# Kernel tuning notes

Measured on AMD Instinct MI355X. Metric: run time of the kernel, lower is better.

The kernel has to match this reference:

```python
import jax, jax.numpy as jnp
import numpy as np

H = 8    # num_heads (per-head feature size after the quirky split)
D_H = 16 # dim_heads (becomes the effective number of heads after split)


def _split_heads(x, B):
    # torch.split(x, H, dim=-1) then cat on dim 0: new_batch = chunk*B + b
    Bt, T, N, D = x.shape
    dh = D // H
    return x.reshape(B, T, N, dh, H).transpose(3, 0, 1, 2, 4).reshape(dh * B, T, N, H)


def _merge_heads(x, B):
    dhB, T, N, Hh = x.shape
    dh = dhB // B
    return x.reshape(dh, B, T, N, Hh).transpose(1, 2, 3, 0, 4).reshape(B, T, N, dh * Hh)


def setup_inputs() -> dict:
    key = jax.random.key(0)
    ks = jax.random.split(key, 10)
    B, T, N, D = 8, 64, 256, 128
    s_in = 1.0 / np.sqrt(2 * D)
    s_d = 1.0 / np.sqrt(D)
    return {
        "X": jax.random.normal(ks[0], (B, T, N, D), jnp.float32),
        "STE": jax.random.normal(ks[1], (B, T, N, D), jnp.float32),
        "Wq": jax.random.normal(ks[2], (2 * D, D), jnp.float32) * s_in,
        "bq": jnp.zeros((D,), jnp.float32),
        "Wk": jax.random.normal(ks[3], (2 * D, D), jnp.float32) * s_in,
        "bk": jnp.zeros((D,), jnp.float32),
        "Wv": jax.random.normal(ks[4], (2 * D, D), jnp.float32) * s_in,
        "bv": jnp.zeros((D,), jnp.float32),
        "Wo": jax.random.normal(ks[5], (D, D), jnp.float32) * s_d,
        "bo": jnp.zeros((D,), jnp.float32),
    }


def reference(X, STE, Wq, bq, Wk, bk, Wv, bv, Wo, bo):
    B, T, N, D = X.shape
    Xc = jnp.concatenate([X, STE], axis=-1)  # [B,T,N,2D]
    Q = jax.nn.relu(Xc @ Wq + bq)
    K = jax.nn.relu(Xc @ Wk + bk)
    V = jax.nn.relu(Xc @ Wv + bv)
    Q = _split_heads(Q, B)  # [dh*B, T, N, H]
    K = _split_heads(K, B)
    V = _split_heads(V, B)
    # scores over time per vertex: [dh*B, N, T, T]
    scores = jnp.einsum("btnh,bsnh->bnts", Q, K) / jnp.sqrt(jnp.float32(D_H))
    causal = jnp.tril(jnp.ones((T, T), bool))
    scores = jnp.where(causal, scores, -jnp.inf)
    attn = jax.nn.softmax(scores, axis=-1)
    out = jnp.einsum("bnts,bsnh->btnh", attn, V)  # [dh*B, T, N, H]
    out = _merge_heads(out, B)  # [B,T,N,D]
    return jax.nn.relu(out @ Wo + bo)
```

## Files before the change

### kernel.cpp

```cpp
#include <hip/hip_runtime.h>

using bf16x8  = __attribute__((ext_vector_type(8))) __bf16;
using f32x4   = __attribute__((ext_vector_type(4))) float;
using short8  = __attribute__((ext_vector_type(8))) short;
using float4v = __attribute__((ext_vector_type(4))) float;
using uint2v  = __attribute__((ext_vector_type(2))) unsigned int;

#if __has_builtin(__builtin_amdgcn_exp2f)
#define EXP2F(x) __builtin_amdgcn_exp2f(x)
#else
#define EXP2F(x) __expf((x) * 0.6931472f)
#endif
#if __has_builtin(__builtin_amdgcn_rcpf)
#define RCPF(x) __builtin_amdgcn_rcpf(x)
#else
#define RCPF(x) (1.f / (x))
#endif

static __device__ __forceinline__ unsigned short bfu(float f) {
    return __builtin_bit_cast(unsigned short, (__bf16)f);
}
static __device__ __forceinline__ unsigned int pkbf(float a, float b) {
    return (unsigned int)bfu(a) | ((unsigned int)bfu(b) << 16);
}
static __device__ __forceinline__ bf16x8 as_bf(short8 s) {
    return __builtin_bit_cast(bf16x8, s);
}

__global__ void prep_weights(const float* __restrict__ Wq, const float* __restrict__ Wk,
                             const float* __restrict__ Wv, const float* __restrict__ Wo,
                             unsigned short* __restrict__ wq2, unsigned short* __restrict__ wo2) {
    int idx = blockIdx.x * 256 + threadIdx.x;
    if (idx < 384 * 256) {
        int c = idx >> 8, k = idx & 255;
        float v = (c < 128) ? Wq[k * 128 + c]
                : (c < 256) ? Wk[k * 128 + (c - 128)]
                            : Wv[k * 128 + (c - 256)];
        wq2[(k >> 5) * 12288 + (c << 5) + (k & 31)] = bfu(v);
    } else {
        int j = idx - 384 * 256;
        int c = j >> 7, k = j & 127;
        wo2[(k >> 5) * 4096 + (c << 5) + (k & 31)] = bfu(Wo[k * 128 + c]);
    }
}

__global__ __launch_bounds__(256, 3)
void fused_attn(const float* __restrict__ X, const float* __restrict__ STE,
                const float* __restrict__ bq, const float* __restrict__ bk,
                const float* __restrict__ bv, const float* __restrict__ bo,
                const unsigned short* __restrict__ wq2, const unsigned short* __restrict__ wo2,
                float* __restrict__ out) {
    __shared__ __align__(16) char sm[49152];
    constexpr int SQ = 0, SK = 16384, SV = 32768;
    const float SC2 = 0.36067376f;

    const int tid  = threadIdx.x;
    const int lane = tid & 63;
    const int w    = tid >> 6;
    const int bid  = blockIdx.x;
    const int n    = bid & 255;
    const int b    = bid >> 8;
    const int lr   = lane & 15;
    const int lg   = lane >> 4;
    const int rsw  = (lr & 7) << 4;

    const size_t base = (size_t)(b * 16384 + n) * 128;
    const float* xbase = X   + base;
    const float* sbase = STE + base;

    const int c0 = w * 96;
    bf16x8 bnxt[6];
    #pragma unroll
    for (int i = 0; i < 6; ++i)
        bnxt[i] = as_bf(*reinterpret_cast<const short8*>(
            wq2 + (size_t)(c0 + i * 16 + lr) * 32 + lg * 8));

    #pragma unroll
    for (int it = 0; it < 16; ++it) {
        int t = w + it * 4;
        const float* src = (lane < 32) ? (xbase + (size_t)t * 32768 + lane * 4)
                                       : (sbase + (size_t)t * 32768 + (lane - 32) * 4);
        float4v v = *reinterpret_cast<const float4v*>(src);
        uint2v d;
        d[0] = pkbf(v[0], v[1]);
        d[1] = pkbf(v[2], v[3]);
        *reinterpret_cast<uint2v*>(sm + (t << 9) + ((lane * 8) ^ ((t & 7) << 4))) = d;
    }
    __syncthreads();

    f32x4 acc[4][6];
    #pragma unroll
    for (int m = 0; m < 4; ++m)
        #pragma unroll
        for (int i = 0; i < 6; ++i)
            acc[m][i] = f32x4{0.f, 0.f, 0.f, 0.f};

    #pragma unroll
    for (int ks = 0; ks < 8; ++ks) {
        bf16x8 bcur[6];
        #pragma unroll
        for (int i = 0; i < 6; ++i) bcur[i] = bnxt[i];
        if (ks < 7) {
            #pragma unroll
            for (int i = 0; i < 6; ++i)
                bnxt[i] = as_bf(*reinterpret_cast<const short8*>(
                    wq2 + (size_t)(ks + 1) * 12288 + (size_t)(c0 + i * 16 + lr) * 32 + lg * 8));
        }
        bf16x8 a[4];
        #pragma unroll
        for (int m = 0; m < 4; ++m)
            a[m] = as_bf(*reinterpret_cast<const short8*>(
                sm + ((m * 16 + lr) << 9) + ((ks * 64 + lg * 16) ^ rsw)));
        #pragma unroll
        for (int m = 0; m < 4; ++m)
            #pragma unroll
            for (int i = 0; i < 6; ++i)
                acc[m][i] = __builtin_amdgcn_mfma_f32_16x16x32_bf16(a[m], bcur[i], acc[m][i], 0, 0, 0);
    }
    __syncthreads();

    #pragma unroll
    for (int i = 0; i < 6; ++i) {
        int c = c0 + i * 16 + lr;
        if (c < 256) {
            int qi = c >> 7, cc = c & 127;
            char* rbase = sm + (qi ? SK : SQ);
            float bvv = (qi ? bk : bq)[cc];
            #pragma unroll
            for (int m = 0; m < 4; ++m)
                #pragma unroll
                for (int r = 0; r < 4; ++r) {
                    int t = m * 16 + lg * 4 + r;
                    *reinterpret_cast<unsigned short*>(
                        rbase + (t << 8) + ((cc * 2) ^ ((t & 7) << 4)))
                        = bfu(fmaxf(acc[m][i][r] + bvv, 0.f));
                }
        } else {
            int cv = c - 256;
            float bvv = bv[cv];
            #pragma unroll
            for (int m = 0; m < 4; ++m) {
                uint2v d;
                d[0] = pkbf(fmaxf(acc[m][i][0] + bvv, 0.f), fmaxf(acc[m][i][1] + bvv, 0.f));
                d[1] = pkbf(fmaxf(acc[m][i][2] + bvv, 0.f), fmaxf(acc[m][i][3] + bvv, 0.f));
                *reinterpret_cast<uint2v*>(
                    sm + SV + (cv << 7) + ((m * 32 + lg * 8) ^ ((cv & 7) << 4))) = d;
            }
        }
    }
    __syncthreads();

    const f32x4 zf = {0.f, 0.f, 0.f, 0.f};
    const short8 z8 = {0, 0, 0, 0, 0, 0, 0, 0};
    short8 ones8;
    #pragma unroll
    for (int h = 0; h < 8; ++h) ones8[h] = (short)0x3F80;

    #pragma unroll 1
    for (int ci = 0; ci < 4; ++ci) {
        const int cb  = (w * 4 + ci) * 8;
        const int cbB = cb * 2;

        bf16x8 kf[4], qf[4];
        #pragma unroll
        for (int j = 0; j < 4; ++j) {
            kf[j] = (lg == 0)
                ? as_bf(*reinterpret_cast<const short8*>(
                      sm + SK + ((j * 16 + lr) << 8) + (cbB ^ rsw)))
                : as_bf(z8);
            qf[j] = (lg == 0)
                ? as_bf(*reinterpret_cast<const short8*>(
                      sm + SQ + ((j * 16 + lr) << 8) + (cbB ^ rsw)))
                : as_bf(z8);
        }
        bf16x8 vf[2];
        #pragma unroll
        for (int ks = 0; ks < 2; ++ks) {
            int vr = min(cb + lr, 127);
            vf[ks] = as_bf(*reinterpret_cast<const short8*>(
                sm + SV + (vr << 7) + ((ks * 64 + lg * 16) ^ ((vr & 7) << 4))));
            if (lr == 8 || lr == 12) vf[ks] = as_bf(ones8);
        }

        #pragma unroll
        for (int nt = 0; nt < 4; ++nt) {
            unsigned int p2[4][2];
            #pragma unroll
            for (int st = 0; st < 4; ++st) {
                if (st > nt) { p2[st][0] = 0; p2[st][1] = 0; continue; }
                f32x4 sv = __builtin_amdgcn_mfma_f32_16x16x32_bf16(kf[st], qf[nt], zf, 0, 0, 0);
                float p[4];
                #pragma unroll
                for (int r = 0; r < 4; ++r) p[r] = EXP2F(sv[r] * SC2);
                if (st == nt) {
                    #pragma unroll
                    for (int r = 0; r < 4; ++r) p[r] = (lg * 4 + r <= lr) ? p[r] : 0.f;
                }
                p2[st][0] = pkbf(p[0], p[1]);
                p2[st][1] = pkbf(p[2], p[3]);
            }

            f32x4 o = zf;
            #pragma unroll
            for (int ks = 0; ks < 2; ++ks) {
                if (nt < 2 * ks) continue;
                unsigned int bw[4];
                #pragma unroll
                for (int q = 0; q < 4; ++q) {
                    int srcl = lr + 16 * (2 * (lg & 1) + (q >> 1));
                    unsigned int v0 = __shfl(p2[2 * ks][q & 1], srcl);
                    unsigned int v1 = __shfl(p2[2 * ks + 1][q & 1], srcl);
                    bw[q] = (lg & 2) ? v1 : v0;
                }
                bf16x8 pf = __builtin_bit_cast(bf16x8, bw);
                o = __builtin_amdgcn_mfma_f32_16x16x32_bf16(vf[ks], pf, o, 0, 0, 0);
            }

            float l   = __shfl_xor(o[0], 32);
            float inv = RCPF(l);
            if (lg < 2) {
                int t_ = nt * 16 + lr;
                uint2v d;
                d[0] = pkbf(o[0] * inv, o[1] * inv);
                d[1] = pkbf(o[2] * inv, o[3] * inv);
                *reinterpret_cast<uint2v*>(
                    sm + SQ + (t_ << 8) + ((cbB + lg * 8) ^ rsw)) = d;
            }
        }
    }
    __syncthreads();

    f32x4 acc2[4][2];
    #pragma unroll
    for (int m = 0; m < 4; ++m)
        #pragma unroll
        for (int i = 0; i < 2; ++i)
            acc2[m][i] = zf;

    #pragma unroll
    for (int ks = 0; ks < 4; ++ks) {
        bf16x8 a2[4];
        #pragma unroll
        for (int m = 0; m < 4; ++m)
            a2[m] = as_bf(*reinterpret_cast<const short8*>(
                sm + SQ + ((m * 16 + lr) << 8) + ((ks * 64 + lg * 16) ^ rsw)));
        bf16x8 b2[2];
        #pragma unroll
        for (int i = 0; i < 2; ++i)
            b2[i] = as_bf(*reinterpret_cast<const short8*>(
                wo2 + (size_t)ks * 4096 + (size_t)((w + 4 * i) * 16 + lr) * 32 + lg * 8));
        #pragma unroll
        for (int m = 0; m < 4; ++m)
            #pragma unroll
            for (int i = 0; i < 2; ++i)
                acc2[m][i] = __builtin_amdgcn_mfma_f32_16x16x32_bf16(a2[m], b2[i], acc2[m][i], 0, 0, 0);
    }

    float* obase = out + base;
    #pragma unroll
    for (int i = 0; i < 2; ++i) {
        int c = (w + 4 * i) * 16 + lr;
        float bias = bo[c];
        #pragma unroll
        for (int m = 0; m < 4; ++m)
            #pragma unroll
            for (int r = 0; r < 4; ++r) {
                int tt = m * 16 + lg * 4 + r;
                obase[(size_t)tt * 32768 + c] = fmaxf(acc2[m][i][r] + bias, 0.f);
            }
    }
}

extern "C" void kernel_launch(void* const* d_in, const int* in_sizes, int n_in,
                              void* d_out, int out_size, void* d_ws, size_t ws_size,
                              hipStream_t stream) {
    const float* X   = (const float*)d_in[0];
    const float* STE = (const float*)d_in[1];
    const float* Wq  = (const float*)d_in[2];
    const float* bq  = (const float*)d_in[3];
    const float* Wk  = (const float*)d_in[4];
    const float* bk  = (const float*)d_in[5];
    const float* Wv  = (const float*)d_in[6];
    const float* bv  = (const float*)d_in[7];
    const float* Wo  = (const float*)d_in[8];
    const float* bo  = (const float*)d_in[9];
    float* out = (float*)d_out;

    unsigned short* wq2 = (unsigned short*)d_ws;
    unsigned short* wo2 = wq2 + 384 * 256;

    prep_weights<<<448, 256, 0, stream>>>(Wq, Wk, Wv, Wo, wq2, wo2);
    fused_attn<<<2048, 256, 0, stream>>>(X, STE, bq, bk, bv, bo, wq2, wo2, out);
}
```

Before: 83.67 us.

## Use 512-thread blocks and split projection and attention work across eight waves

Doubles the workgroup to 8 waves per (batch, vertex) block. The QKV projection tile is split by row half and column third, attention chunks are halved per wave, and the output projection gives each wave one 16-column slice. The explicit prefetch of the next weight tile into registers is dropped in favour of direct loads inside the loop. The aim is more waves in flight to hide memory latency and fewer registers per wave, at the cost of losing the software prefetch and doing more redundant weight loads per block.

```diff
diff --git a/kernel.cpp b/kernel.cpp
--- a/kernel.cpp
+++ b/kernel.cpp
@@ -44,7 +44,7 @@
     }
 }
 
-__global__ __launch_bounds__(256, 3)
+__global__ __launch_bounds__(512, 6)
 void fused_attn(const float* __restrict__ X, const float* __restrict__ STE,
                 const float* __restrict__ bq, const float* __restrict__ bk,
                 const float* __restrict__ bv, const float* __restrict__ bo,
@@ -68,16 +68,9 @@
     const float* xbase = X   + base;
     const float* sbase = STE + base;
 
-    const int c0 = w * 96;
-    bf16x8 bnxt[6];
-    #pragma unroll
-    for (int i = 0; i < 6; ++i)
-        bnxt[i] = as_bf(*reinterpret_cast<const short8*>(
-            wq2 + (size_t)(c0 + i * 16 + lr) * 32 + lg * 8));
-
-    #pragma unroll
-    for (int it = 0; it < 16; ++it) {
-        int t = w + it * 4;
+    #pragma unroll
+    for (int it = 0; it < 8; ++it) {
+        int t = w + it * 8;
         const float* src = (lane < 32) ? (xbase + (size_t)t * 32768 + lane * 4)
                                        : (sbase + (size_t)t * 32768 + (lane - 32) * 4);
         float4v v = *reinterpret_cast<const float4v*>(src);
@@ -88,34 +81,34 @@
     }
     __syncthreads();
 
-    f32x4 acc[4][6];
-    #pragma unroll
-    for (int m = 0; m < 4; ++m)
+    const int mh = (w & 1) * 32;
+    const int c0 = (w >> 1) * 96;
+    f32x4 acc[2][6];
+    #pragma unroll
+    for (int m = 0; m < 2; ++m)
         #pragma unroll
         for (int i = 0; i < 6; ++i)
             acc[m][i] = f32x4{0.f, 0.f, 0.f, 0.f};
 
     #pragma unroll
     for (int ks = 0; ks < 8; ++ks) {
-        bf16x8 bcur[6];
-        #pragma unroll
-        for (int i = 0; i < 6; ++i) bcur[i] = bnxt[i];
-        if (ks < 7) {
-            #pragma unroll
-            for (int i = 0; i < 6; ++i)
-                bnxt[i] = as_bf(*reinterpret_cast<const short8*>(
-                    wq2 + (size_t)(ks + 1) * 12288 + (size_t)(c0 + i * 16 + lr) * 32 + lg * 8));
-        }
-        bf16x8 a[4];
-        #pragma unroll
-        for (int m = 0; m < 4; ++m)
-            a[m] = as_bf(*reinterpret_cast<const short8*>(
-                sm + ((m * 16 + lr) << 9) + ((ks * 64 + lg * 16) ^ rsw)));
-        #pragma unroll
-        for (int m = 0; m < 4; ++m)
-            #pragma unroll
-            for (int i = 0; i < 6; ++i)
-                acc[m][i] = __builtin_amdgcn_mfma_f32_16x16x32_bf16(a[m], bcur[i], acc[m][i], 0, 0, 0);
+        bf16x8 a0 = as_bf(*reinterpret_cast<const short8*>(
+            sm + ((mh + lr) << 9) + ((ks * 64 + lg * 16) ^ rsw)));
+        bf16x8 a1 = as_bf(*reinterpret_cast<const short8*>(
+            sm + ((mh + 16 + lr) << 9) + ((ks * 64 + lg * 16) ^ rsw)));
+        #pragma unroll
+        for (int h = 0; h < 2; ++h) {
+            bf16x8 bt[3];
+            #pragma unroll
+            for (int j = 0; j < 3; ++j)
+                bt[j] = as_bf(*reinterpret_cast<const short8*>(
+                    wq2 + (size_t)ks * 12288 + (size_t)(c0 + (h * 3 + j) * 16 + lr) * 32 + lg * 8));
+            #pragma unroll
+            for (int j = 0; j < 3; ++j) {
+                acc[0][h * 3 + j] = __builtin_amdgcn_mfma_f32_16x16x32_bf16(a0, bt[j], acc[0][h * 3 + j], 0, 0, 0);
+                acc[1][h * 3 + j] = __builtin_amdgcn_mfma_f32_16x16x32_bf16(a1, bt[j], acc[1][h * 3 + j], 0, 0, 0);
+            }
+        }
     }
     __syncthreads();
 
@@ -127,10 +120,10 @@
             char* rbase = sm + (qi ? SK : SQ);
             float bvv = (qi ? bk : bq)[cc];
             #pragma unroll
-            for (int m = 0; m < 4; ++m)
+            for (int m = 0; m < 2; ++m)
                 #pragma unroll
                 for (int r = 0; r < 4; ++r) {
-                    int t = m * 16 + lg * 4 + r;
+                    int t = mh + m * 16 + lg * 4 + r;
                     *reinterpret_cast<unsigned short*>(
                         rbase + (t << 8) + ((cc * 2) ^ ((t & 7) << 4)))
                         = bfu(fmaxf(acc[m][i][r] + bvv, 0.f));
@@ -139,12 +132,12 @@
             int cv = c - 256;
             float bvv = bv[cv];
             #pragma unroll
-            for (int m = 0; m < 4; ++m) {
+            for (int m = 0; m < 2; ++m) {
                 uint2v d;
                 d[0] = pkbf(fmaxf(acc[m][i][0] + bvv, 0.f), fmaxf(acc[m][i][1] + bvv, 0.f));
                 d[1] = pkbf(fmaxf(acc[m][i][2] + bvv, 0.f), fmaxf(acc[m][i][3] + bvv, 0.f));
                 *reinterpret_cast<uint2v*>(
-                    sm + SV + (cv << 7) + ((m * 32 + lg * 8) ^ ((cv & 7) << 4))) = d;
+                    sm + SV + (cv << 7) + ((2 * mh + m * 32 + lg * 8) ^ ((cv & 7) << 4))) = d;
             }
         }
     }
@@ -157,8 +150,8 @@
     for (int h = 0; h < 8; ++h) ones8[h] = (short)0x3F80;
 
     #pragma unroll 1
-    for (int ci = 0; ci < 4; ++ci) {
-        const int cb  = (w * 4 + ci) * 8;
+    for (int ci = 0; ci < 2; ++ci) {
+        const int cb  = (w * 2 + ci) * 8;
         const int cbB = cb * 2;
 
         bf16x8 kf[4], qf[4];
@@ -230,43 +223,29 @@
     }
     __syncthreads();
 
-    f32x4 acc2[4][2];
-    #pragma unroll
-    for (int m = 0; m < 4; ++m)
-        #pragma unroll
-        for (int i = 0; i < 2; ++i)
-            acc2[m][i] = zf;
-
+    f32x4 acc2[4] = {zf, zf, zf, zf};
     #pragma unroll
     for (int ks = 0; ks < 4; ++ks) {
-        bf16x8 a2[4];
-        #pragma unroll
-        for (int m = 0; m < 4; ++m)
-            a2[m] = as_bf(*reinterpret_cast<const short8*>(
+        bf16x8 b2 = as_bf(*reinterpret_cast<const short8*>(
+            wo2 + (size_t)ks * 4096 + (size_t)(w * 16 + lr) * 32 + lg * 8));
+        #pragma unroll
+        for (int m = 0; m < 4; ++m) {
+            bf16x8 a2 = as_bf(*reinterpret_cast<const short8*>(
                 sm + SQ + ((m * 16 + lr) << 8) + ((ks * 64 + lg * 16) ^ rsw)));
-        bf16x8 b2[2];
-        #pragma unroll
-        for (int i = 0; i < 2; ++i)
-            b2[i] = as_bf(*reinterpret_cast<const short8*>(
-                wo2 + (size_t)ks * 4096 + (size_t)((w + 4 * i) * 16 + lr) * 32 + lg * 8));
-        #pragma unroll
-        for (int m = 0; m < 4; ++m)
-            #pragma unroll
-            for (int i = 0; i < 2; ++i)
-                acc2[m][i] = __builtin_amdgcn_mfma_f32_16x16x32_bf16(a2[m], b2[i], acc2[m][i], 0, 0, 0);
+            acc2[m] = __builtin_amdgcn_mfma_f32_16x16x32_bf16(a2, b2, acc2[m], 0, 0, 0);
+        }
     }
 
     float* obase = out + base;
-    #pragma unroll
-    for (int i = 0; i < 2; ++i) {
-        int c = (w + 4 * i) * 16 + lr;
+    {
+        int c = w * 16 + lr;
         float bias = bo[c];
         #pragma unroll
         for (int m = 0; m < 4; ++m)
             #pragma unroll
             for (int r = 0; r < 4; ++r) {
                 int tt = m * 16 + lg * 4 + r;
-                obase[(size_t)tt * 32768 + c] = fmaxf(acc2[m][i][r] + bias, 0.f);
+                obase[(size_t)tt * 32768 + c] = fmaxf(acc2[m][r] + bias, 0.f);
             }
     }
 }
@@ -290,5 +269,5 @@
     unsigned short* wo2 = wq2 + 384 * 256;
 
     prep_weights<<<448, 256, 0, stream>>>(Wq, Wk, Wv, Wo, wq2, wo2);
-    fused_attn<<<2048, 256, 0, stream>>>(X, STE, bq, bk, bv, bo, wq2, wo2, out);
-}
+    fused_attn<<<2048, 512, 0, stream>>>(X, STE, bq, bk, bv, bo, wq2, wo2, out);
+}
```

Measured after the change: 106.0 us. 26.7% more time.
